# Kernel optimization log

Hardware: AMD Instinct MI355X
Metric: run time of the kernel (lower is better)

Reference implementation:

```python
import jax, jax.numpy as jnp
import numpy as np

TEMP = 0.05


def setup_inputs() -> dict:
    key = jax.random.key(0)
    k1, k2, k3 = jax.random.split(key, 3)
    B, D, NC = 1024, 256, 50000  # batch, feat dim, num clusters
    inputs = jax.random.normal(k1, (B, D), dtype=jnp.float32)
    targets = jax.random.randint(k2, (B,), 0, NC, dtype=jnp.int64)
    feats = jax.random.normal(k3, (2 * NC, D), dtype=jnp.float32)
    # memory bank rows are kept L2-normalized by the module's update rule
    feats = feats / jnp.linalg.norm(feats, axis=1, keepdims=True)
    return {"inputs": inputs, "targets": targets, "features": feats}


def reference(inputs, targets, features):
    # F.normalize(inputs, dim=1)
    x = inputs / jnp.linalg.norm(inputs, axis=1, keepdims=True)
    # outputs = x @ features.T / temp  -> [B, 2*NC]
    logits = jnp.matmul(x, features.T) / TEMP
    mean_logits, hard_logits = jnp.split(logits, 2, axis=1)  # each [B, NC]

    def ce(lg):
        logp = jax.nn.log_softmax(lg, axis=1)
        return -jnp.take_along_axis(logp, targets[:, None], axis=1).mean()

    loss = 0.5 * (ce(hard_logits) + ce(mean_logits))
    return loss
```

## Files before the change

### kernel.cpp

```cpp
#include <hip/hip_runtime.h>
#include <math.h>

#define BATCH 1024
#define DIM   256
#define NCL   50000
#define TOTC  100000
#define NSLICE 16
#define K2E   28.853900817779268f

typedef __attribute__((ext_vector_type(8)))  short bf16x8;
typedef __attribute__((ext_vector_type(16))) float f32x16;

__device__ __forceinline__ unsigned int f2bf(float f) {
    unsigned int u = __float_as_uint(f);
    return (u + 0x7FFFu + ((u >> 16) & 1u)) >> 16;
}

__global__ __launch_bounds__(64) void k_prep(const float* __restrict__ in,
                                             const int* __restrict__ tgt,
                                             const float* __restrict__ feats,
                                             unsigned short* __restrict__ xnT,
                                             float* __restrict__ Sx,
                                             float* __restrict__ z) {
    const int b = blockIdx.x;
    const int t = threadIdx.x;
    float4 v = *(const float4*)&in[b * DIM + t * 4];
    float ss = v.x * v.x + v.y * v.y + v.z * v.z + v.w * v.w;
#pragma unroll
    for (int o = 1; o < 64; o <<= 1) ss += __shfl_xor(ss, o, 64);
    const float sc = 1.0f / sqrtf(ss);
    float4 w;
    w.x = v.x * sc; w.y = v.y * sc; w.z = v.z * sc; w.w = v.w * sc;

    uint2 p;
    p.x = f2bf(w.x * K2E) | (f2bf(w.y * K2E) << 16);
    p.y = f2bf(w.z * K2E) | (f2bf(w.w * K2E) << 16);
    *(uint2*)((char*)xnT + (t >> 1) * 16384 + b * 16 + (t & 1) * 8) = p;

    const int tb = tgt[b];
#pragma unroll
    for (int h = 0; h < 2; ++h) {
        const int row = tb + h * NCL;
        float4 f = *(const float4*)&feats[row * DIM + t * 4];
        float d = w.x * f.x + w.y * f.y + w.z * f.z + w.w * f.w;
#pragma unroll
        for (int o = 1; o < 64; o <<= 1) d += __shfl_xor(d, o, 64);
        if (t == 0) z[b * 2 + h] = d * 20.0f;
    }
    if (t < 32) Sx[b * 32 + t] = 0.0f;
}

__global__ __launch_bounds__(256, 3) void k_main(const unsigned short* __restrict__ xnT,
                                                 const float* __restrict__ feats,
                                                 float* __restrict__ Sx) {
    __shared__ unsigned short Ab[64 * 256];

    const int tid  = threadIdx.x;
    const int lane = tid & 63;
    const int wn   = tid >> 6;
    const int l31  = lane & 31;
    const int hi   = lane >> 5;
    const int cb0  = blockIdx.x * 64;
    float* Ss = Sx + (blockIdx.x & (NSLICE - 1)) * (BATCH * 2);

#pragma unroll
    for (int it = 0; it < 8; ++it) {
        const int idx = it * 256 + tid;
        const int r = idx >> 5;
        const int c = idx & 31;
        int gr = cb0 + r;
        if (gr > TOTC - 1) gr = TOTC - 1;
        const float4 f0 = *(const float4*)&feats[(size_t)gr * DIM + c * 8];
        const float4 f1 = *(const float4*)&feats[(size_t)gr * DIM + c * 8 + 4];
        uint4 pk;
        pk.x = f2bf(f0.x) | (f2bf(f0.y) << 16);
        pk.y = f2bf(f0.z) | (f2bf(f0.w) << 16);
        pk.z = f2bf(f1.x) | (f2bf(f1.y) << 16);
        pk.w = f2bf(f1.z) | (f2bf(f1.w) << 16);
        *(uint4*)((char*)Ab + c * 1024 + ((r * 16) ^ ((c & 7) << 4))) = pk;
    }
    __syncthreads();

    const bool mixed = (cb0 < NCL && cb0 + 63 >= NCL) || (cb0 + 63 >= TOTC);
    const int  halfsel = (cb0 >= NCL) ? 1 : 0;

    float sr0[4][2], sr1[4][2];

#pragma unroll
    for (int p = 0; p < 4; ++p) {
        const unsigned short* bb0 = xnT + (size_t)hi * 8192
                                  + (size_t)(p * 256 + wn * 64 + l31) * 8;
        const unsigned short* bb1 = bb0 + 256;

        f32x16 acc[2][2];
#pragma unroll
        for (int mt = 0; mt < 2; ++mt) {
            acc[mt][0] = (f32x16)(0.0f);
            acc[mt][1] = (f32x16)(0.0f);
        }

        __builtin_amdgcn_s_setprio(1);
#pragma unroll
        for (int kk = 0; kk < 16; ++kk) {
            const bf16x8 b0 = *(const bf16x8*)(bb0 + (size_t)kk * 16384);
            const bf16x8 b1 = *(const bf16x8*)(bb1 + (size_t)kk * 16384);
            const int ch = kk * 2 + hi;
            const int kbase = ch * 1024;
            const int key = (ch & 7) << 4;
#pragma unroll
            for (int mt = 0; mt < 2; ++mt) {
                const bf16x8 a = *(const bf16x8*)((const char*)Ab + kbase
                                   + ((mt * 512 + l31 * 16) ^ key));
                acc[mt][0] = __builtin_amdgcn_mfma_f32_32x32x16_bf16(a, b0, acc[mt][0], 0, 0, 0);
                acc[mt][1] = __builtin_amdgcn_mfma_f32_32x32x16_bf16(a, b1, acc[mt][1], 0, 0, 0);
            }
        }
        __builtin_amdgcn_s_setprio(0);

        if (!mixed) {
#pragma unroll
            for (int nn = 0; nn < 2; ++nn) {
                float sa = 0.0f, sb = 0.0f;
#pragma unroll
                for (int r = 0; r < 16; ++r) {
                    sa += exp2f(acc[0][nn][r]);
                    sb += exp2f(acc[1][nn][r]);
                }
                float s = sa + sb;
                s += __shfl_xor(s, 32, 64);
                sr0[p][nn] = s;
                sr1[p][nn] = 0.0f;
            }
        } else {
#pragma unroll
            for (int nn = 0; nn < 2; ++nn) {
                float sh0 = 0.0f, sh1 = 0.0f;
#pragma unroll
                for (int mt = 0; mt < 2; ++mt)
#pragma unroll
                    for (int r = 0; r < 16; ++r) {
                        const int cl = cb0 + mt * 32 +
                                       (r & 3) + 8 * (r >> 2) + 4 * hi;
                        const bool valid = cl < TOTC;
                        float e = exp2f(acc[mt][nn][r]);
                        e = valid ? e : 0.0f;
                        sh0 += (cl < NCL) ? e : 0.0f;
                        sh1 += (cl < NCL) ? 0.0f : e;
                    }
                sh0 += __shfl_xor(sh0, 32, 64);
                sh1 += __shfl_xor(sh1, 32, 64);
                sr0[p][nn] = sh0;
                sr1[p][nn] = sh1;
            }
        }
    }

    if (hi == 0) {
#pragma unroll
        for (int p = 0; p < 4; ++p)
#pragma unroll
            for (int nn = 0; nn < 2; ++nn) {
                const int col = p * 256 + wn * 64 + nn * 32 + l31;
                if (!mixed) {
                    atomicAdd(&Ss[col * 2 + halfsel], sr0[p][nn]);
                } else {
                    atomicAdd(&Ss[col * 2 + 0], sr0[p][nn]);
                    atomicAdd(&Ss[col * 2 + 1], sr1[p][nn]);
                }
            }
    }
}

__global__ __launch_bounds__(256) void k_loss(const float* __restrict__ Sx,
                                              const float* __restrict__ z,
                                              float* __restrict__ out) {
    const int t = threadIdx.x;
    float part = 0.0f;
    for (int r = t; r < BATCH; r += 256) {
        float s0 = 0.0f, s1 = 0.0f;
#pragma unroll
        for (int sl = 0; sl < NSLICE; ++sl) {
            s0 += Sx[sl * (BATCH * 2) + r * 2 + 0];
            s1 += Sx[sl * (BATCH * 2) + r * 2 + 1];
        }
        part += logf(s0) + logf(s1) - z[r * 2 + 0] - z[r * 2 + 1];
    }
#pragma unroll
    for (int o = 1; o < 64; o <<= 1) part += __shfl_xor(part, o, 64);
    __shared__ float ws[4];
    if ((t & 63) == 0) ws[t >> 6] = part;
    __syncthreads();
    if (t == 0) {
        const float tot = ws[0] + ws[1] + ws[2] + ws[3];
        out[0] = 0.5f * tot / (float)BATCH;
    }
}

extern "C" void kernel_launch(void* const* d_in, const int* in_sizes, int n_in,
                              void* d_out, int out_size, void* d_ws, size_t ws_size,
                              hipStream_t stream) {
    const float* inputs  = (const float*)d_in[0];
    const int*   targets = (const int*)d_in[1];
    const float* feats   = (const float*)d_in[2];
    float* out = (float*)d_out;

    unsigned short* xnT = (unsigned short*)d_ws;
    float* Sx = (float*)(xnT + BATCH * DIM);
    float* zt = Sx + NSLICE * BATCH * 2;

    k_prep<<<BATCH, 64, 0, stream>>>(inputs, targets, feats, xnT, Sx, zt);
    const int nblk = (TOTC + 63) / 64;
    k_main<<<nblk, 256, 0, stream>>>(xnT, feats, Sx);
    k_loss<<<1, 256, 0, stream>>>(Sx, zt, out);
}
```

Before: 98.42 us.

## Software-pipeline B global loads and A LDS reads in main MFMA loop

Rewrites the inner MFMA loop of k_main to prefetch the x (B operand) fragments four k-steps ahead in a rotating register ring that runs across column passes, and to double-buffer the LDS A-fragment reads one step ahead. It also removes the s_setprio hints and drops the occupancy hint of 3 from launch_bounds. The aim is to hide global and LDS latency behind MFMA issue. The cost is extra registers, which together with the relaxed launch bounds may lower occupancy.

```diff
diff --git a/kernel.cpp b/kernel.cpp
--- a/kernel.cpp
+++ b/kernel.cpp
@@ -50,9 +50,9 @@
     if (t < 32) Sx[b * 32 + t] = 0.0f;
 }
 
-__global__ __launch_bounds__(256, 3) void k_main(const unsigned short* __restrict__ xnT,
-                                                 const float* __restrict__ feats,
-                                                 float* __restrict__ Sx) {
+__global__ __launch_bounds__(256) void k_main(const unsigned short* __restrict__ xnT,
+                                              const float* __restrict__ feats,
+                                              float* __restrict__ Sx) {
     __shared__ unsigned short Ab[64 * 256];
 
     const int tid  = threadIdx.x;
@@ -84,13 +84,25 @@
     const bool mixed = (cb0 < NCL && cb0 + 63 >= NCL) || (cb0 + 63 >= TOTC);
     const int  halfsel = (cb0 >= NCL) ? 1 : 0;
 
+#define LDA(mt_, kv_) (*(const bf16x8*)((const char*)Ab + ((kv_)*2 + hi) * 1024 \
+                        + ((((mt_)*512) + l31*16) ^ (((((kv_)*2 + hi)) & 7) << 4))))
+
+    const unsigned short* bp0 = xnT + (size_t)hi * 8192 + (size_t)(wn * 64 + l31) * 8;
+    const unsigned short* bp1 = bp0 + 256;
+
     float sr0[4][2], sr1[4][2];
 
+    bf16x8 q0[4], q1[4];
+#pragma unroll
+    for (int i = 0; i < 4; ++i) {
+        q0[i] = *(const bf16x8*)(bp0 + (size_t)i * 16384);
+        q1[i] = *(const bf16x8*)(bp1 + (size_t)i * 16384);
+    }
+
 #pragma unroll
     for (int p = 0; p < 4; ++p) {
-        const unsigned short* bb0 = xnT + (size_t)hi * 8192
-                                  + (size_t)(p * 256 + wn * 64 + l31) * 8;
-        const unsigned short* bb1 = bb0 + 256;
+        const unsigned short* bc0 = bp0 + (size_t)p * 2048;
+        const unsigned short* bc1 = bp1 + (size_t)p * 2048;
 
         f32x16 acc[2][2];
 #pragma unroll
@@ -99,23 +111,31 @@
             acc[mt][1] = (f32x16)(0.0f);
         }
 
-        __builtin_amdgcn_s_setprio(1);
+        bf16x8 a0c = LDA(0, 0);
+        bf16x8 a1c = LDA(1, 0);
+
 #pragma unroll
         for (int kk = 0; kk < 16; ++kk) {
-            const bf16x8 b0 = *(const bf16x8*)(bb0 + (size_t)kk * 16384);
-            const bf16x8 b1 = *(const bf16x8*)(bb1 + (size_t)kk * 16384);
-            const int ch = kk * 2 + hi;
-            const int kbase = ch * 1024;
-            const int key = (ch & 7) << 4;
-#pragma unroll
-            for (int mt = 0; mt < 2; ++mt) {
-                const bf16x8 a = *(const bf16x8*)((const char*)Ab + kbase
-                                   + ((mt * 512 + l31 * 16) ^ key));
-                acc[mt][0] = __builtin_amdgcn_mfma_f32_32x32x16_bf16(a, b0, acc[mt][0], 0, 0, 0);
-                acc[mt][1] = __builtin_amdgcn_mfma_f32_32x32x16_bf16(a, b1, acc[mt][1], 0, 0, 0);
-            }
-        }
-        __builtin_amdgcn_s_setprio(0);
+            const bf16x8 b0 = q0[kk & 3];
+            const bf16x8 b1 = q1[kk & 3];
+            bf16x8 a0n, a1n;
+            if (kk < 15) {
+                a0n = LDA(0, kk + 1);
+                a1n = LDA(1, kk + 1);
+            }
+            if (kk < 12) {
+                q0[kk & 3] = *(const bf16x8*)(bc0 + (size_t)(kk + 4) * 16384);
+                q1[kk & 3] = *(const bf16x8*)(bc1 + (size_t)(kk + 4) * 16384);
+            } else if (p < 3) {
+                q0[kk & 3] = *(const bf16x8*)(bc0 + 2048 + (size_t)(kk - 12) * 16384);
+                q1[kk & 3] = *(const bf16x8*)(bc1 + 2048 + (size_t)(kk - 12) * 16384);
+            }
+            acc[0][0] = __builtin_amdgcn_mfma_f32_32x32x16_bf16(a0c, b0, acc[0][0], 0, 0, 0);
+            acc[0][1] = __builtin_amdgcn_mfma_f32_32x32x16_bf16(a0c, b1, acc[0][1], 0, 0, 0);
+            acc[1][0] = __builtin_amdgcn_mfma_f32_32x32x16_bf16(a1c, b0, acc[1][0], 0, 0, 0);
+            acc[1][1] = __builtin_amdgcn_mfma_f32_32x32x16_bf16(a1c, b1, acc[1][1], 0, 0, 0);
+            if (kk < 15) { a0c = a0n; a1c = a1n; }
+        }
 
         if (!mixed) {
 #pragma unroll
@@ -154,6 +174,7 @@
             }
         }
     }
+#undef LDA
 
     if (hi == 0) {
 #pragma unroll
```

After: 141.9 us. 1.44x slower.
